# Optimization experiments

Hardware: AMD Instinct MI355X
Metric: run time of the kernel (lower is better)

The kernel has to match this reference:

```python
import jax, jax.numpy as jnp
import numpy as np

M = 128  # split point: first M units use max-plus, rest use min-plus

def setup_inputs() -> dict:
    key = jax.random.key(0)
    k1, k2 = jax.random.split(key)
    x = jax.random.normal(k1, (2048, 512), dtype=jnp.float32)   # (batch, features_in)
    w = jax.random.normal(k2, (512, 256), dtype=jnp.float32)    # (features_in, units)
    return {"x": x, "w": w}

def reference(x, w):
    # Tropical (max/min-plus) pseudo-matmul.
    # s[b, f, u] = x[b, f] + w[f, u]; reduce over f.
    s_max = x[:, :, None] + w[None, :, :M]          # (batch, f, M)
    s_min = x[:, :, None] + w[None, :, M:]          # (batch, f, units-M)
    hv = jnp.max(s_max, axis=1)                     # (batch, M)
    hw = jnp.min(s_min, axis=1)                     # (batch, units-M)
    return jnp.concatenate([hv, hw], axis=1)        # linear activation = identity
```

## Files before the change

### kernel.cpp

```cpp
#include <hip/hip_runtime.h>
#include <math.h>


#define FEAT  512
#define UNITS 256
#define BR    4
#define KW    64
#define NW    8

__device__ __forceinline__ float max3(float a, float b, float c) {
    return fmaxf(fmaxf(a, b), c);
}

__global__ __launch_bounds__(512, 2) void tropical_kernel(const float* __restrict__ x,
                                                          const float* __restrict__ w,
                                                          float* __restrict__ out) {
    __shared__ float lds[NW * BR * UNITS];
    const int tid  = threadIdx.x;
    const int lane = tid & 63;
    const int wv   = __builtin_amdgcn_readfirstlane(tid >> 6);
    const int u0   = lane * 4;
    const float sgn = (lane < 32) ? 1.0f : -1.0f;
    const int row0 = blockIdx.x * BR;
    const int kb   = wv * KW;

    {
        const float4* src = (const float4*)(x + (size_t)row0 * FEAT);
        ((float4*)lds)[tid] = src[tid];
    }

    const float* wp = w + (size_t)kb * UNITS + u0;

    float4 acc[BR];
    #pragma unroll
    for (int r = 0; r < BR; ++r)
        acc[r] = make_float4(-__builtin_inff(), -__builtin_inff(),
                             -__builtin_inff(), -__builtin_inff());

    __syncthreads();

    #pragma unroll 1
    for (int q = 0; q < KW / 4; ++q) {
        float4 wq[4];
        #pragma unroll
        for (int k = 0; k < 4; ++k)
            wq[k] = *(const float4*)(wp + (size_t)(q * 4 + k) * UNITS);

        const float4 w0 = make_float4(wq[0].x*sgn, wq[0].y*sgn, wq[0].z*sgn, wq[0].w*sgn);
        const float4 w1 = make_float4(wq[1].x*sgn, wq[1].y*sgn, wq[1].z*sgn, wq[1].w*sgn);
        const float4 w2 = make_float4(wq[2].x*sgn, wq[2].y*sgn, wq[2].z*sgn, wq[2].w*sgn);
        const float4 w3 = make_float4(wq[3].x*sgn, wq[3].y*sgn, wq[3].z*sgn, wq[3].w*sgn);

        #pragma unroll
        for (int r = 0; r < BR; ++r) {
            const float4 a = *(const float4*)&lds[r * FEAT + kb + q * 4];
            float4 A = acc[r];
            A.x = max3(A.x, fmaf(a.x, sgn, w0.x), fmaf(a.y, sgn, w1.x));
            A.x = max3(A.x, fmaf(a.z, sgn, w2.x), fmaf(a.w, sgn, w3.x));
            A.y = max3(A.y, fmaf(a.x, sgn, w0.y), fmaf(a.y, sgn, w1.y));
            A.y = max3(A.y, fmaf(a.z, sgn, w2.y), fmaf(a.w, sgn, w3.y));
            A.z = max3(A.z, fmaf(a.x, sgn, w0.z), fmaf(a.y, sgn, w1.z));
            A.z = max3(A.z, fmaf(a.z, sgn, w2.z), fmaf(a.w, sgn, w3.z));
            A.w = max3(A.w, fmaf(a.x, sgn, w0.w), fmaf(a.y, sgn, w1.w));
            A.w = max3(A.w, fmaf(a.z, sgn, w2.w), fmaf(a.w, sgn, w3.w));
            acc[r] = A;
        }
    }

    __syncthreads();
    #pragma unroll
    for (int r = 0; r < BR; ++r)
        *(float4*)&lds[((wv * BR + r) * UNITS) + u0] = acc[r];
    __syncthreads();

    const int r   = tid >> 7;
    const int up0 = (tid & 127) * 2;
    float2 v = *(const float2*)&lds[(0 * BR + r) * UNITS + up0];
    #pragma unroll
    for (int j = 1; j < NW; ++j) {
        const float2 p = *(const float2*)&lds[(j * BR + r) * UNITS + up0];
        v.x = fmaxf(v.x, p.x);
        v.y = fmaxf(v.y, p.y);
    }
    const float so = (up0 < 128) ? 1.0f : -1.0f;
    *(float2*)&out[(size_t)(row0 + r) * UNITS + up0] = make_float2(v.x * so, v.y * so);
}

extern "C" void kernel_launch(void* const* d_in, const int* in_sizes, int n_in,
                              void* d_out, int out_size, void* d_ws, size_t ws_size,
                              hipStream_t stream) {
    const float* x = (const float*)d_in[0];
    const float* w = (const float*)d_in[1];
    float* out = (float*)d_out;

    tropical_kernel<<<dim3(2048 / BR), dim3(512), 0, stream>>>(x, w, out);
}
```

Baseline: 68.41 us.

## Double the rows per block and software-pipeline the W and x loads

Each block now handles 8 batch rows instead of 4, so every W quad loaded from global memory is reused across twice as many rows, and the grid shrinks to half as many blocks. The inner loop is double-buffered: the next W and x quads are loaded into registers while the current quad is computed. The final reduction moves to float4 accesses. The costs are more registers and twice the LDS per block (64 KB), and dropping the two-blocks-per-CU launch bound may lower occupancy.

```diff
diff --git a/kernel.cpp b/kernel.cpp
--- a/kernel.cpp
+++ b/kernel.cpp
@@ -4,17 +4,55 @@
 
 #define FEAT  512
 #define UNITS 256
-#define BR    4
+#define BR    8
 #define KW    64
 #define NW    8
+#define NQ    (KW / 4)
 
 __device__ __forceinline__ float max3(float a, float b, float c) {
     return fmaxf(fmaxf(a, b), c);
 }
 
-__global__ __launch_bounds__(512, 2) void tropical_kernel(const float* __restrict__ x,
-                                                          const float* __restrict__ w,
-                                                          float* __restrict__ out) {
+__device__ __forceinline__ void load_xquad(const float* __restrict__ lds, int kb, int q,
+                                           float4* __restrict__ xb) {
+    #pragma unroll
+    for (int r = 0; r < BR; ++r)
+        xb[r] = *(const float4*)&lds[r * FEAT + kb + q * 4];
+}
+
+__device__ __forceinline__ void load_wquad(const float* __restrict__ wp, int q,
+                                           float4* __restrict__ wb) {
+    #pragma unroll
+    for (int k = 0; k < 4; ++k)
+        wb[k] = *(const float4*)(wp + (size_t)(q * 4 + k) * UNITS);
+}
+
+__device__ __forceinline__ void compute_quad(const float4* __restrict__ xb,
+                                             const float4* __restrict__ wq,
+                                             float sgn, float4* __restrict__ acc) {
+    const float4 w0 = make_float4(wq[0].x*sgn, wq[0].y*sgn, wq[0].z*sgn, wq[0].w*sgn);
+    const float4 w1 = make_float4(wq[1].x*sgn, wq[1].y*sgn, wq[1].z*sgn, wq[1].w*sgn);
+    const float4 w2 = make_float4(wq[2].x*sgn, wq[2].y*sgn, wq[2].z*sgn, wq[2].w*sgn);
+    const float4 w3 = make_float4(wq[3].x*sgn, wq[3].y*sgn, wq[3].z*sgn, wq[3].w*sgn);
+    #pragma unroll
+    for (int r = 0; r < BR; ++r) {
+        const float4 a = xb[r];
+        float4 A = acc[r];
+        A.x = max3(A.x, fmaf(a.x, sgn, w0.x), fmaf(a.y, sgn, w1.x));
+        A.x = max3(A.x, fmaf(a.z, sgn, w2.x), fmaf(a.w, sgn, w3.x));
+        A.y = max3(A.y, fmaf(a.x, sgn, w0.y), fmaf(a.y, sgn, w1.y));
+        A.y = max3(A.y, fmaf(a.z, sgn, w2.y), fmaf(a.w, sgn, w3.y));
+        A.z = max3(A.z, fmaf(a.x, sgn, w0.z), fmaf(a.y, sgn, w1.z));
+        A.z = max3(A.z, fmaf(a.z, sgn, w2.z), fmaf(a.w, sgn, w3.z));
+        A.w = max3(A.w, fmaf(a.x, sgn, w0.w), fmaf(a.y, sgn, w1.w));
+        A.w = max3(A.w, fmaf(a.z, sgn, w2.w), fmaf(a.w, sgn, w3.w));
+        acc[r] = A;
+    }
+}
+
+__global__ __launch_bounds__(512) void tropical_kernel(const float* __restrict__ x,
+                                                       const float* __restrict__ w,
+                                                       float* __restrict__ out) {
     __shared__ float lds[NW * BR * UNITS];
     const int tid  = threadIdx.x;
     const int lane = tid & 63;
@@ -26,7 +64,8 @@
 
     {
         const float4* src = (const float4*)(x + (size_t)row0 * FEAT);
-        ((float4*)lds)[tid] = src[tid];
+        ((float4*)lds)[tid]       = src[tid];
+        ((float4*)lds)[tid + 512] = src[tid + 512];
     }
 
     const float* wp = w + (size_t)kb * UNITS + u0;
@@ -37,34 +76,22 @@
         acc[r] = make_float4(-__builtin_inff(), -__builtin_inff(),
                              -__builtin_inff(), -__builtin_inff());
 
+    float4 xA[BR], xB[BR], wA[4], wB[4];
+    load_wquad(wp, 0, wA);
+
     __syncthreads();
+    load_xquad(lds, kb, 0, xA);
 
     #pragma unroll 1
-    for (int q = 0; q < KW / 4; ++q) {
-        float4 wq[4];
-        #pragma unroll
-        for (int k = 0; k < 4; ++k)
-            wq[k] = *(const float4*)(wp + (size_t)(q * 4 + k) * UNITS);
-
-        const float4 w0 = make_float4(wq[0].x*sgn, wq[0].y*sgn, wq[0].z*sgn, wq[0].w*sgn);
-        const float4 w1 = make_float4(wq[1].x*sgn, wq[1].y*sgn, wq[1].z*sgn, wq[1].w*sgn);
-        const float4 w2 = make_float4(wq[2].x*sgn, wq[2].y*sgn, wq[2].z*sgn, wq[2].w*sgn);
-        const float4 w3 = make_float4(wq[3].x*sgn, wq[3].y*sgn, wq[3].z*sgn, wq[3].w*sgn);
-
-        #pragma unroll
-        for (int r = 0; r < BR; ++r) {
-            const float4 a = *(const float4*)&lds[r * FEAT + kb + q * 4];
-            float4 A = acc[r];
-            A.x = max3(A.x, fmaf(a.x, sgn, w0.x), fmaf(a.y, sgn, w1.x));
-            A.x = max3(A.x, fmaf(a.z, sgn, w2.x), fmaf(a.w, sgn, w3.x));
-            A.y = max3(A.y, fmaf(a.x, sgn, w0.y), fmaf(a.y, sgn, w1.y));
-            A.y = max3(A.y, fmaf(a.z, sgn, w2.y), fmaf(a.w, sgn, w3.y));
-            A.z = max3(A.z, fmaf(a.x, sgn, w0.z), fmaf(a.y, sgn, w1.z));
-            A.z = max3(A.z, fmaf(a.z, sgn, w2.z), fmaf(a.w, sgn, w3.z));
-            A.w = max3(A.w, fmaf(a.x, sgn, w0.w), fmaf(a.y, sgn, w1.w));
-            A.w = max3(A.w, fmaf(a.z, sgn, w2.w), fmaf(a.w, sgn, w3.w));
-            acc[r] = A;
+    for (int q = 0; q < NQ; q += 2) {
+        load_wquad(wp, q + 1, wB);
+        load_xquad(lds, kb, q + 1, xB);
+        compute_quad(xA, wA, sgn, acc);
+        if (q + 2 < NQ) {
+            load_wquad(wp, q + 2, wA);
+            load_xquad(lds, kb, q + 2, xA);
         }
+        compute_quad(xB, wB, sgn, acc);
     }
 
     __syncthreads();
@@ -73,17 +100,20 @@
         *(float4*)&lds[((wv * BR + r) * UNITS) + u0] = acc[r];
     __syncthreads();
 
-    const int r   = tid >> 7;
-    const int up0 = (tid & 127) * 2;
-    float2 v = *(const float2*)&lds[(0 * BR + r) * UNITS + up0];
+    const int r  = tid >> 6;
+    const int uo = (tid & 63) * 4;
+    float4 v = *(const float4*)&lds[(0 * BR + r) * UNITS + uo];
     #pragma unroll
     for (int j = 1; j < NW; ++j) {
-        const float2 p = *(const float2*)&lds[(j * BR + r) * UNITS + up0];
+        const float4 p = *(const float4*)&lds[(j * BR + r) * UNITS + uo];
         v.x = fmaxf(v.x, p.x);
         v.y = fmaxf(v.y, p.y);
+        v.z = fmaxf(v.z, p.z);
+        v.w = fmaxf(v.w, p.w);
     }
-    const float so = (up0 < 128) ? 1.0f : -1.0f;
-    *(float2*)&out[(size_t)(row0 + r) * UNITS + up0] = make_float2(v.x * so, v.y * so);
+    const float so = (uo < 128) ? 1.0f : -1.0f;
+    *(float4*)&out[(size_t)(row0 + r) * UNITS + uo] =
+        make_float4(v.x * so, v.y * so, v.z * so, v.w * so);
 }
 
 extern "C" void kernel_launch(void* const* d_in, const int* in_sizes, int n_in,
```

New measurement: 67.70 us (median of 2 runs). About the same (-1.0%).
